# Optimization experiments

Hardware: AMD Instinct MI355X
Metric: run time of the kernel (lower is better)

Reference implementation:

```python
import jax, jax.numpy as jnp
import numpy as np

N = 50000
E = 800000
R = 8
F_IN = 128
H = 128          # num_hidden
F_OUT = 128      # num_outputs
D1, D2, D3 = 2 * H, H, F_OUT


def _glorot(key, shape):
    fan_in, fan_out = shape[-2], shape[-1]
    lim = np.sqrt(6.0 / (fan_in + fan_out)).astype(np.float32)
    return jax.random.uniform(key, shape, jnp.float32, -lim, lim)


def setup_inputs() -> dict:
    key = jax.random.key(0)
    ks = jax.random.split(key, 12)
    x = jax.random.normal(ks[0], (N, F_IN), jnp.float32)
    edge_index = jax.random.randint(ks[1], (2, E), 0, N, jnp.int64)
    edge_type = jax.random.randint(ks[2], (E,), 0, R, jnp.int64)
    return {
        "x": x,
        "edge_index": edge_index,
        "edge_type": edge_type,
        "w1": _glorot(ks[3], (R, F_IN, D1)),
        "root1": _glorot(ks[4], (F_IN, D1)),
        "b1": jnp.zeros((D1,), jnp.float32),
        "w2": _glorot(ks[5], (R, D1, D2)),
        "root2": _glorot(ks[6], (D1, D2)),
        "b2": jnp.zeros((D2,), jnp.float32),
        "w3": _glorot(ks[7], (R, D2, D3)),
        "root3": _glorot(ks[8], (D2, D3)),
        "b3": jnp.zeros((D3,), jnp.float32),
    }


def _rgcn_layer(h, src, dst, seg, inv_cnt, W, root, bias):
    # Per-relation mean aggregation via a fused (dst, rel) segment id,
    # then a grouped contraction with the per-relation weights.
    n, fin = h.shape
    s = jax.ops.segment_sum(h[src], seg, num_segments=n * R)  # [N*R, fin]
    agg = s.reshape(n, R, fin) * inv_cnt                      # mean per (node, rel)
    return jnp.einsum("nri,rio->no", agg, W) + h @ root + bias


def reference(x, edge_index, edge_type, w1, root1, b1, w2, root2, b2, w3, root3, b3):
    src, dst = edge_index[0], edge_index[1]
    seg = dst * R + edge_type                                  # fused (dst, rel) id
    cnt = jax.ops.segment_sum(jnp.ones((E,), x.dtype), seg, num_segments=N * R)
    inv_cnt = (1.0 / jnp.maximum(cnt, 1.0)).reshape(N, R, 1)

    h1 = jax.nn.elu(_rgcn_layer(x, src, dst, seg, inv_cnt, w1, root1, b1))
    # dropout: identity (eval mode)
    h2 = jax.nn.elu(_rgcn_layer(h1, src, dst, seg, inv_cnt, w2, root2, b2))
    h3 = jax.nn.elu(_rgcn_layer(h2, src, dst, seg, inv_cnt, w3, root3, b3))
    return jnp.concatenate([h1, h2, h3], axis=1)               # [N, D1+D2+D3]
```

## Files before the change

kernel.cpp:

```cpp
#include <hip/hip_runtime.h>


#define DEVI __device__ __forceinline__

constexpr int NN    = 50000;
constexpr int EE    = 800000;
constexpr int RREL  = 8;
constexpr int NRSEG = NN * RREL;
constexpr int NTC   = 1152;

using u16 = unsigned short;
using u32 = unsigned int;
using u64 = unsigned long long;

typedef short short8 __attribute__((ext_vector_type(8)));
typedef float f32x4  __attribute__((ext_vector_type(4)));

DEVI float bf2f(u32 u){ union{u32 i; float f;} x; x.i = u << 16; return x.f; }
DEVI u16   f2b(float f){ u32 u = __float_as_uint(f); u32 r = u + 0x7fffu + ((u >> 16) & 1u); return (u16)(r >> 16); }

typedef const __attribute__((address_space(1))) u32 gas_u32;
typedef __attribute__((address_space(3))) u32       las_u32;
DEVI void gload16(const void* g, void* l){
  __builtin_amdgcn_global_load_lds((gas_u32*)(u64)g, (las_u32*)(u64)l, 16, 0, 0);
}


__global__ void count_k(const int* __restrict__ dst, const int* __restrict__ et, int* __restrict__ cnt){
  int e = blockIdx.x * 256 + threadIdx.x;
  if(e < EE) atomicAdd(&cnt[dst[e] * RREL + et[e]], 1);
}

constexpr int SCAN_E = 8;
constexpr int CHUNK  = 2048;
constexpr int NB     = (NRSEG + CHUNK - 1) / CHUNK;

__global__ void scan1_k(const int* __restrict__ cnt, int* __restrict__ bsums){
  __shared__ int sm[256];
  int b = blockIdx.x, t = threadIdx.x;
  int base = b * CHUNK + t * SCAN_E;
  int s = 0;
  #pragma unroll
  for(int j = 0; j < SCAN_E; j++){ int i = base + j; s += (i < NRSEG) ? cnt[i] : 0; }
  sm[t] = s; __syncthreads();
  for(int off = 128; off > 0; off >>= 1){ if(t < off) sm[t] += sm[t + off]; __syncthreads(); }
  if(t == 0) bsums[b] = sm[0];
}

__global__ void scan2_k(int* __restrict__ bsums){
  __shared__ int sm[256];
  int t = threadIdx.x;
  int v = (t < NB) ? bsums[t] : 0;
  sm[t] = v; __syncthreads();
  for(int off = 1; off < 256; off <<= 1){
    int x = (t >= off) ? sm[t - off] : 0; __syncthreads();
    sm[t] += x; __syncthreads();
  }
  if(t < NB) bsums[t] = sm[t] - v;
}

__global__ void scan3_k(const int* __restrict__ cnt, const int* __restrict__ bsums, int* __restrict__ offs){
  __shared__ int sm[256];
  int b = blockIdx.x, t = threadIdx.x;
  int base = b * CHUNK + t * SCAN_E;
  int loc[SCAN_E]; int run = 0;
  #pragma unroll
  for(int j = 0; j < SCAN_E; j++){ int i = base + j; int c = (i < NRSEG) ? cnt[i] : 0; loc[j] = run; run += c; }
  sm[t] = run; __syncthreads();
  for(int off = 1; off < 256; off <<= 1){
    int x = (t >= off) ? sm[t - off] : 0; __syncthreads();
    sm[t] += x; __syncthreads();
  }
  int tb = bsums[b] + sm[t] - run;
  #pragma unroll
  for(int j = 0; j < SCAN_E; j++){ int i = base + j; if(i < NRSEG) offs[i] = tb + loc[j]; }
  if(b == 0 && t == 0) offs[NRSEG] = EE;
}

__global__ void inv_k(const int* __restrict__ cnt, float* __restrict__ inv){
  int i = blockIdx.x * 256 + threadIdx.x;
  if(i < NRSEG){ int c = cnt[i]; inv[i] = 1.0f / (float)(c > 0 ? c : 1); }
}

__global__ void fill_k(const int* __restrict__ src, const int* __restrict__ dst, const int* __restrict__ et,
                       const int* __restrict__ offs, int* __restrict__ fill, int* __restrict__ spk){
  int e = blockIdx.x * 256 + threadIdx.x;
  if(e < EE){
    int d = dst[e], r = et[e];
    int seg = d * RREL + r;
    int i = atomicAdd(&fill[seg], 1);
    spk[offs[seg] + i] = (src[e] << 3) | r;
  }
}

__global__ void castx_k(const float* __restrict__ x, u16* __restrict__ xb){
  int i = blockIdx.x * 256 + threadIdx.x;
  if(i < NN * 128) xb[i] = f2b(x[i]);
}

__global__ void packw_k(const float* __restrict__ w, const float* __restrict__ root,
                        u16* __restrict__ wp, int FIN, int FOUT){
  int idx = blockIdx.x * 256 + threadIdx.x;
  int tot = (RREL + 1) * FIN * FOUT;
  if(idx < tot){
    int i = idx % FIN;
    int o = (idx / FIN) % FOUT;
    int g = idx / (FIN * FOUT);
    float v = (g < RREL) ? w[((size_t)g * FIN + i) * FOUT + o] : root[(size_t)i * FOUT + o];
    wp[idx] = f2b(v);
  }
}


DEVI void acc8(float* a, uint4 v){
  a[0] += bf2f(v.x & 0xffffu); a[1] += bf2f(v.x >> 16);
  a[2] += bf2f(v.y & 0xffffu); a[3] += bf2f(v.y >> 16);
  a[4] += bf2f(v.z & 0xffffu); a[5] += bf2f(v.z >> 16);
  a[6] += bf2f(v.w & 0xffffu); a[7] += bf2f(v.w >> 16);
}

DEVI void fma8(float* a, uint4 v, float c){
  a[0] += c * bf2f(v.x & 0xffffu); a[1] += c * bf2f(v.x >> 16);
  a[2] += c * bf2f(v.y & 0xffffu); a[3] += c * bf2f(v.y >> 16);
  a[4] += c * bf2f(v.z & 0xffffu); a[5] += c * bf2f(v.z >> 16);
  a[6] += c * bf2f(v.w & 0xffffu); a[7] += c * bf2f(v.w >> 16);
}

template<int FIN, int RSUB>
__global__ __launch_bounds__(256)
void agg_k(const u16* __restrict__ hb, const int* __restrict__ spk,
           const int* __restrict__ offs, const float* __restrict__ inv,
           u16* __restrict__ agg, int r0)
{
  constexpr int G   = FIN / 8;
  constexpr int LDW = RSUB * FIN;
  const int gl  = threadIdx.x & (G - 1);
  int gid = (int)((blockIdx.x * blockDim.x + threadIdx.x) / G);
  const int ng = (int)((gridDim.x * blockDim.x) / G);
  const int S = NN * RSUB;
  for(int s = gid; s < S; s += ng){
    int n = s / RSUB, rr = s - n * RSUB;
    int seg = n * RREL + r0 + rr;
    int beg = offs[seg], end = offs[seg + 1];
    float sc = inv[seg];
    float acc[8];
    #pragma unroll
    for(int i = 0; i < 8; i++) acc[i] = 0.f;
    int e = beg;
    for(; e + 2 <= end; e += 2){
      int s0 = spk[e] >> 3, s1 = spk[e + 1] >> 3;
      uint4 v0 = ((const uint4*)(hb + (size_t)s0 * FIN))[gl];
      uint4 v1 = ((const uint4*)(hb + (size_t)s1 * FIN))[gl];
      acc8(acc, v0);
      acc8(acc, v1);
    }
    if(e < end){
      uint4 v0 = ((const uint4*)(hb + (size_t)(spk[e] >> 3) * FIN))[gl];
      acc8(acc, v0);
    }
    uint4 o;
    o.x = (u32)f2b(acc[0] * sc) | ((u32)f2b(acc[1] * sc) << 16);
    o.y = (u32)f2b(acc[2] * sc) | ((u32)f2b(acc[3] * sc) << 16);
    o.z = (u32)f2b(acc[4] * sc) | ((u32)f2b(acc[5] * sc) << 16);
    o.w = (u32)f2b(acc[6] * sc) | ((u32)f2b(acc[7] * sc) << 16);
    ((uint4*)(agg + (size_t)n * LDW + rr * FIN))[gl] = o;
  }
}


template<int FIN, int NAGG, bool ROOT, int FOUT>
__global__ __launch_bounds__(512)
void gemm_k(const u16* __restrict__ Aagg, const u16* __restrict__ Aroot,
            const u16* __restrict__ Wagg, const u16* __restrict__ Wroot,
            const float* __restrict__ bias, float* __restrict__ dout,
            u16* __restrict__ hbout)
{
  static_assert(FIN % 32 == 0, "");
  constexpr int KSG = FIN / 32;
  constexpr int NG  = NAGG + (ROOT ? 1 : 0);
  constexpr int NKS = NG * KSG;
  constexpr int LDA = NAGG * FIN;
  constexpr int WN    = (FOUT == 256) ? 4 : 2;
  constexpr int WM    = 8 / WN;
  constexpr int WROWS = 128 / WM;
  constexpr int MREP  = WROWS / 16;
  constexpr int ASL = 512;
  constexpr int BSL = FOUT * 4;
  __shared__ u16 lds[2][(ASL + BSL) * 8];
  const int bm  = (int)blockIdx.x;
  const int tid = threadIdx.x;
  const int wid = tid >> 6, lane = tid & 63;
  const int wm  = wid / WN, wn = wid % WN;

  auto stage = [&](int ks, u16* l){
    u16* lA = l;
    u16* lB = l + ASL * 8;
    int g    = ks / KSG;
    int koff = (ks - g * KSG) * 32;
    bool isRoot = ROOT && (g == NAGG);
    {
      int sb = wid * 64;
      int s  = sb + lane;
      int pair = s >> 3, cs = s & 7;
      int c    = cs ^ (pair & 7);
      int row  = pair * 2 + (c >> 2);
      int k8   = c & 3;
      int kk   = koff + k8 * 8;
      int rowg = bm * 128 + row; rowg = rowg < NN ? rowg : NN - 1;
      const u16* ga = isRoot ? (Aroot + (size_t)rowg * FIN + kk)
                             : (Aagg + (size_t)rowg * LDA + g * FIN + kk);
      gload16(ga, lA + sb * 8);
    }
    #pragma unroll
    for(int rnd = 0; rnd < BSL / 512; rnd++){
      int sb = rnd * 512 + wid * 64;
      int s  = sb + lane;
      int pair = s >> 3, cs = s & 7;
      int c    = cs ^ (pair & 7);
      int row  = pair * 2 + (c >> 2);
      int k8   = c & 3;
      int kk   = koff + k8 * 8;
      const u16* gb = isRoot ? (Wroot + (size_t)row * FIN + kk)
                             : (Wagg + ((size_t)g * FOUT + row) * FIN + kk);
      gload16(gb, lB + sb * 8);
    }
  };

  auto ldfrag = [&](const u16* buf, int row, int k8){
    int pair = row >> 1;
    int c    = ((row & 1) << 2) + k8;
    int cs   = c ^ (pair & 7);
    return *(const short8*)(buf + pair * 64 + cs * 8);
  };

  f32x4 acc[MREP][4] = {};

  stage(0, (u16*)lds[0]);
  __syncthreads();
  for(int ks = 0; ks < NKS; ks++){
    int cur = ks & 1;
    if(ks + 1 < NKS) stage(ks + 1, (u16*)lds[cur ^ 1]);
    const u16* lA = (const u16*)lds[cur];
    const u16* lB = lA + ASL * 8;
    short8 af[MREP], bf4[4];
    #pragma unroll
    for(int m = 0; m < MREP; m++) af[m] = ldfrag(lA, wm * WROWS + m * 16 + (lane & 15), lane >> 4);
    #pragma unroll
    for(int n = 0; n < 4; n++) bf4[n] = ldfrag(lB, wn * 64 + n * 16 + (lane & 15), lane >> 4);
    #pragma unroll
    for(int m = 0; m < MREP; m++)
      #pragma unroll
      for(int n = 0; n < 4; n++)
        acc[m][n] = __builtin_amdgcn_mfma_f32_16x16x32_bf16(af[m], bf4[n], acc[m][n], 0, 0, 0);
    __syncthreads();
  }

  #pragma unroll
  for(int m = 0; m < MREP; m++){
    #pragma unroll
    for(int j = 0; j < 4; j++){
      int grow = bm * 128 + wm * WROWS + m * 16 + (lane >> 4) * 4 + j;
      if(grow >= NN) continue;
      #pragma unroll
      for(int n = 0; n < 4; n++){
        int gcol = wn * 64 + n * 16 + (lane & 15);
        float v = acc[m][n][j];
        v += bias[gcol];
        v = v > 0.f ? v : expm1f(v);
        dout[(size_t)grow * 512 + gcol] = v;
        if(hbout) hbout[(size_t)grow * FOUT + gcol] = f2b(v);
      }
    }
  }
}


template<int FIN>
__global__ __launch_bounds__(512)
void dgemm_k(const u16* __restrict__ A, const u16* __restrict__ Bw, u16* __restrict__ T)
{
  constexpr int NKS = FIN / 32;
  constexpr int ASL = 512;
  constexpr int BSL = 512;
  constexpr int LPS = 2;
  __shared__ u16 lds[3][(ASL + BSL) * 8];
  const int bid = (int)blockIdx.x;
  const int bm  = bid / 9;
  const int jc  = bid % 9;
  const int tid = threadIdx.x;
  const int wid = tid >> 6, lane = tid & 63;
  const int wm  = wid >> 1, wn = wid & 1;

  auto stage = [&](int ks, u16* l){
    u16* lA = l;
    u16* lB = l + ASL * 8;
    int koff = ks * 32;
    {
      int sb = wid * 64;
      int s  = sb + lane;
      int pair = s >> 3, cs = s & 7;
      int c    = cs ^ (pair & 7);
      int row  = pair * 2 + (c >> 2);
      int k8   = c & 3;
      int kk   = koff + k8 * 8;
      int rowg = bm * 128 + row; rowg = rowg < NN ? rowg : NN - 1;
      gload16(A + (size_t)rowg * FIN + kk, lA + sb * 8);
    }
    {
      int sb = wid * 64;
      int s  = sb + lane;
      int pair = s >> 3, cs = s & 7;
      int c    = cs ^ (pair & 7);
      int row  = pair * 2 + (c >> 2);
      int k8   = c & 3;
      int kk   = koff + k8 * 8;
      gload16(Bw + ((size_t)(jc * 128 + row)) * FIN + kk, lB + sb * 8);
    }
  };

  auto ldfrag = [&](const u16* buf, int row, int k8){
    int pair = row >> 1;
    int c    = ((row & 1) << 2) + k8;
    int cs   = c ^ (pair & 7);
    return *(const short8*)(buf + pair * 64 + cs * 8);
  };

  f32x4 acc[2][4] = {};

  stage(0, (u16*)lds[0]);
  stage(1, (u16*)lds[1]);
  for(int ks = 0; ks < NKS; ks++){
    if(ks + 1 < NKS){
      asm volatile("s_waitcnt vmcnt(%0)" :: "i"(LPS) : "memory");
    } else {
      asm volatile("s_waitcnt vmcnt(0)" ::: "memory");
    }
    __builtin_amdgcn_sched_barrier(0);
    __builtin_amdgcn_s_barrier();
    __builtin_amdgcn_sched_barrier(0);
    if(ks + 2 < NKS) stage(ks + 2, (u16*)lds[(ks + 2) % 3]);
    const u16* lA = (const u16*)lds[ks % 3];
    const u16* lB = lA + ASL * 8;
    short8 af[2], bf4[4];
    #pragma unroll
    for(int m = 0; m < 2; m++) af[m] = ldfrag(lA, wm * 32 + m * 16 + (lane & 15), lane >> 4);
    #pragma unroll
    for(int n = 0; n < 4; n++) bf4[n] = ldfrag(lB, wn * 64 + n * 16 + (lane & 15), lane >> 4);
    #pragma unroll
    for(int m = 0; m < 2; m++)
      #pragma unroll
      for(int n = 0; n < 4; n++)
        acc[m][n] = __builtin_amdgcn_mfma_f32_16x16x32_bf16(af[m], bf4[n], acc[m][n], 0, 0, 0);
  }

  #pragma unroll
  for(int m = 0; m < 2; m++){
    #pragma unroll
    for(int j = 0; j < 4; j++){
      int grow = bm * 128 + wm * 32 + m * 16 + (lane >> 4) * 4 + j;
      if(grow >= NN) continue;
      #pragma unroll
      for(int n = 0; n < 4; n++){
        int gcol = wn * 64 + n * 16 + (lane & 15);
        T[(size_t)grow * NTC + jc * 128 + gcol] = f2b(acc[m][n][j]);
      }
    }
  }
}


template<bool HB>
__global__ __launch_bounds__(256)
void scat_k(const u16* __restrict__ T, const int* __restrict__ spk,
            const int* __restrict__ offs, const float* __restrict__ inv,
            const float* __restrict__ bias, float* __restrict__ dout, int dcol0,
            u16* __restrict__ hbout)
{
  const int gl = threadIdx.x & 15;
  int n = (int)((blockIdx.x * 256 + threadIdx.x) >> 4);
  if(n >= NN) return;
  const float* invn = inv + n * RREL;
  float acc[8];
  {
    uint4 v = *(const uint4*)(T + (size_t)n * NTC + 1024 + gl * 8);
    acc[0] = bf2f(v.x & 0xffffu); acc[1] = bf2f(v.x >> 16);
    acc[2] = bf2f(v.y & 0xffffu); acc[3] = bf2f(v.y >> 16);
    acc[4] = bf2f(v.z & 0xffffu); acc[5] = bf2f(v.z >> 16);
    acc[6] = bf2f(v.w & 0xffffu); acc[7] = bf2f(v.w >> 16);
  }
  int e  = offs[n * RREL];
  int e1 = offs[n * RREL + RREL];
  for(; e + 8 <= e1; e += 8){
    int p[8];
    #pragma unroll
    for(int j = 0; j < 8; j++) p[j] = spk[e + j];
    uint4 v[8];
    #pragma unroll
    for(int j = 0; j < 8; j++)
      v[j] = *(const uint4*)(T + (size_t)(p[j] >> 3) * NTC + (p[j] & 7) * 128 + gl * 8);
    #pragma unroll
    for(int j = 0; j < 8; j++) fma8(acc, v[j], invn[p[j] & 7]);
  }
  for(; e + 4 <= e1; e += 4){
    int p0 = spk[e], p1 = spk[e + 1], p2 = spk[e + 2], p3 = spk[e + 3];
    uint4 v0 = *(const uint4*)(T + (size_t)(p0 >> 3) * NTC + (p0 & 7) * 128 + gl * 8);
    uint4 v1 = *(const uint4*)(T + (size_t)(p1 >> 3) * NTC + (p1 & 7) * 128 + gl * 8);
    uint4 v2 = *(const uint4*)(T + (size_t)(p2 >> 3) * NTC + (p2 & 7) * 128 + gl * 8);
    uint4 v3 = *(const uint4*)(T + (size_t)(p3 >> 3) * NTC + (p3 & 7) * 128 + gl * 8);
    fma8(acc, v0, invn[p0 & 7]); fma8(acc, v1, invn[p1 & 7]);
    fma8(acc, v2, invn[p2 & 7]); fma8(acc, v3, invn[p3 & 7]);
  }
  for(; e < e1; e++){
    int p0 = spk[e];
    uint4 v0 = *(const uint4*)(T + (size_t)(p0 >> 3) * NTC + (p0 & 7) * 128 + gl * 8);
    fma8(acc, v0, invn[p0 & 7]);
  }
  float o[8];
  #pragma unroll
  for(int i = 0; i < 8; i++){
    float v = acc[i] + bias[gl * 8 + i];
    o[i] = v > 0.f ? v : expm1f(v);
  }
  float4* dp = (float4*)(dout + (size_t)n * 512 + dcol0 + gl * 8);
  dp[0] = make_float4(o[0], o[1], o[2], o[3]);
  dp[1] = make_float4(o[4], o[5], o[6], o[7]);
  if(HB){
    uint4 hv;
    hv.x = (u32)f2b(o[0]) | ((u32)f2b(o[1]) << 16);
    hv.y = (u32)f2b(o[2]) | ((u32)f2b(o[3]) << 16);
    hv.z = (u32)f2b(o[4]) | ((u32)f2b(o[5]) << 16);
    hv.w = (u32)f2b(o[6]) | ((u32)f2b(o[7]) << 16);
    *(uint4*)(hbout + (size_t)n * 128 + gl * 8) = hv;
  }
}


extern "C" void kernel_launch(void* const* d_in, const int* in_sizes, int n_in,
                              void* d_out, int out_size, void* d_ws, size_t ws_size,
                              hipStream_t stream)
{
  const float* x     = (const float*)d_in[0];
  const int*   ei    = (const int*)d_in[1];
  const int*   et    = (const int*)d_in[2];
  const float* w1    = (const float*)d_in[3];
  const float* root1 = (const float*)d_in[4];
  const float* b1    = (const float*)d_in[5];
  const float* w2    = (const float*)d_in[6];
  const float* root2 = (const float*)d_in[7];
  const float* b2    = (const float*)d_in[8];
  const float* w3    = (const float*)d_in[9];
  const float* root3 = (const float*)d_in[10];
  const float* b3    = (const float*)d_in[11];
  float* out = (float*)d_out;

  const int* esrc = ei;
  const int* edst = ei + EE;

  char* w = (char*)d_ws;
  auto alloc = [&](size_t bytes)->char*{ char* p = w; w += (bytes + 255) & ~(size_t)255; return p; };
  int*   cnt   = (int*)  alloc((size_t)NRSEG * 4);
  int*   offs  = (int*)  alloc((size_t)(NRSEG + 1) * 4);
  int*   fill  = (int*)  alloc((size_t)NRSEG * 4);
  float* inv   = (float*)alloc((size_t)NRSEG * 4);
  int*   spk   = (int*)  alloc((size_t)EE * 4);
  u16*   xb    = (u16*)  alloc((size_t)NN * 128 * 2);
  u16*   h1b   = (u16*)  alloc((size_t)NN * 256 * 2);
  u16*   h2b   = (u16*)  alloc((size_t)NN * 128 * 2);
  u16*   wp1   = (u16*)  alloc((size_t)9 * 256 * 128 * 2);
  u16*   wp2   = (u16*)  alloc((size_t)9 * 256 * 128 * 2);
  u16*   wp3   = (u16*)  alloc((size_t)9 * 128 * 128 * 2);
  int*   bsums = (int*)  alloc(1024 * 4);
  u16*   agg   = (u16*)  alloc((size_t)NN * 1024 * 2);
  u16*   T     = (u16*)  alloc((size_t)NN * NTC * 2);
  (void)ws_size; (void)in_sizes; (void)n_in; (void)out_size;

  hipMemsetAsync(cnt,  0, (size_t)NRSEG * 4, stream);
  hipMemsetAsync(fill, 0, (size_t)NRSEG * 4, stream);

  count_k<<<(EE + 255) / 256, 256, 0, stream>>>(edst, et, cnt);
  scan1_k<<<NB, 256, 0, stream>>>(cnt, bsums);
  scan2_k<<<1, 256, 0, stream>>>(bsums);
  scan3_k<<<NB, 256, 0, stream>>>(cnt, bsums, offs);
  inv_k<<<(NRSEG + 255) / 256, 256, 0, stream>>>(cnt, inv);
  fill_k<<<(EE + 255) / 256, 256, 0, stream>>>(esrc, edst, et, offs, fill, spk);
  castx_k<<<(NN * 128 + 255) / 256, 256, 0, stream>>>(x, xb);

  packw_k<<<(9 * 128 * 256 + 255) / 256, 256, 0, stream>>>(w1, root1, wp1, 128, 256);
  packw_k<<<(9 * 256 * 128 + 255) / 256, 256, 0, stream>>>(w2, root2, wp2, 256, 128);
  packw_k<<<(9 * 128 * 128 + 255) / 256, 256, 0, stream>>>(w3, root3, wp3, 128, 128);

  const int MT = (NN + 127) / 128;
  const int SB = (NN * 16 + 255) / 256;

  agg_k<128, 8><<<4096, 256, 0, stream>>>(xb, spk, offs, inv, agg, 0);
  gemm_k<128, 8, true, 256><<<MT, 512, 0, stream>>>(
      agg, xb, wp1, wp1 + (size_t)8 * 256 * 128, b1, out + 0, h1b);

  dgemm_k<256><<<MT * 9, 512, 0, stream>>>(h1b, wp2, T);
  scat_k<true><<<SB, 256, 0, stream>>>(T, spk, offs, inv, b2, out, 256, h2b);

  dgemm_k<128><<<MT * 9, 512, 0, stream>>>(h2b, wp3, T);
  scat_k<false><<<SB, 256, 0, stream>>>(T, spk, offs, inv, b3, out, 384, nullptr);
}
```

Before: 422.1 us.

## Fold root into aggregated buffer and reuse split-column dgemm for layer one

Layer one now packs the root features alongside the eight relation aggregates in a single K=1152 row buffer. Its weights are packed into one matching matrix. The dedicated full-width gemm kernel is replaced by the existing pipelined dgemm kernel, split into two 128-column blocks per row tile, with a bias/ELU epilogue. This raises the block count and uses the triple-buffered pipeline, at the cost of reading the A tile twice and an extra strided write of x into the aggregate buffer.

```diff
diff --git a/kernel.cpp b/kernel.cpp
--- a/kernel.cpp
+++ b/kernel.cpp
@@ -93,9 +93,14 @@
   }
 }
 
-__global__ void castx_k(const float* __restrict__ x, u16* __restrict__ xb){
+__global__ void castx_k(const float* __restrict__ x, u16* __restrict__ xb, u16* __restrict__ agg2){
   int i = blockIdx.x * 256 + threadIdx.x;
-  if(i < NN * 128) xb[i] = f2b(x[i]);
+  if(i < NN * 128){
+    u16 v = f2b(x[i]);
+    xb[i] = v;
+    int n = i >> 7, c = i & 127;
+    agg2[(size_t)n * NTC + 1024 + c] = v;
+  }
 }
 
 __global__ void packw_k(const float* __restrict__ w, const float* __restrict__ root,
@@ -111,6 +116,16 @@
   }
 }
 
+__global__ void packw1_k(const float* __restrict__ w, const float* __restrict__ root, u16* __restrict__ wp){
+  int idx = blockIdx.x * 256 + threadIdx.x;
+  if(idx < 256 * NTC){
+    int o = idx / NTC, k = idx % NTC;
+    int g = k >> 7, i = k & 127;
+    float v = (g < RREL) ? w[((size_t)g * 128 + i) * 256 + o] : root[(size_t)i * 256 + o];
+    wp[idx] = f2b(v);
+  }
+}
+
 
 DEVI void acc8(float* a, uint4 v){
   a[0] += bf2f(v.x & 0xffffu); a[1] += bf2f(v.x >> 16);
@@ -126,14 +141,13 @@
   a[6] += c * bf2f(v.w & 0xffffu); a[7] += c * bf2f(v.w >> 16);
 }
 
-template<int FIN, int RSUB>
+template<int FIN, int RSUB, int LDW>
 __global__ __launch_bounds__(256)
 void agg_k(const u16* __restrict__ hb, const int* __restrict__ spk,
            const int* __restrict__ offs, const float* __restrict__ inv,
            u16* __restrict__ agg, int r0)
 {
-  constexpr int G   = FIN / 8;
-  constexpr int LDW = RSUB * FIN;
+  constexpr int G = FIN / 8;
   const int gl  = threadIdx.x & (G - 1);
   int gid = (int)((blockIdx.x * blockDim.x + threadIdx.x) / G);
   const int ng = (int)((gridDim.x * blockDim.x) / G);
@@ -168,125 +182,20 @@
 }
 
 
-template<int FIN, int NAGG, bool ROOT, int FOUT>
+template<int K, int NJC, int EPI>
 __global__ __launch_bounds__(512)
-void gemm_k(const u16* __restrict__ Aagg, const u16* __restrict__ Aroot,
-            const u16* __restrict__ Wagg, const u16* __restrict__ Wroot,
-            const float* __restrict__ bias, float* __restrict__ dout,
-            u16* __restrict__ hbout)
+void dgemm_k(const u16* __restrict__ A, const u16* __restrict__ Bw,
+             u16* __restrict__ T, const float* __restrict__ bias,
+             float* __restrict__ dout, u16* __restrict__ hbout)
 {
-  static_assert(FIN % 32 == 0, "");
-  constexpr int KSG = FIN / 32;
-  constexpr int NG  = NAGG + (ROOT ? 1 : 0);
-  constexpr int NKS = NG * KSG;
-  constexpr int LDA = NAGG * FIN;
-  constexpr int WN    = (FOUT == 256) ? 4 : 2;
-  constexpr int WM    = 8 / WN;
-  constexpr int WROWS = 128 / WM;
-  constexpr int MREP  = WROWS / 16;
-  constexpr int ASL = 512;
-  constexpr int BSL = FOUT * 4;
-  __shared__ u16 lds[2][(ASL + BSL) * 8];
-  const int bm  = (int)blockIdx.x;
-  const int tid = threadIdx.x;
-  const int wid = tid >> 6, lane = tid & 63;
-  const int wm  = wid / WN, wn = wid % WN;
-
-  auto stage = [&](int ks, u16* l){
-    u16* lA = l;
-    u16* lB = l + ASL * 8;
-    int g    = ks / KSG;
-    int koff = (ks - g * KSG) * 32;
-    bool isRoot = ROOT && (g == NAGG);
-    {
-      int sb = wid * 64;
-      int s  = sb + lane;
-      int pair = s >> 3, cs = s & 7;
-      int c    = cs ^ (pair & 7);
-      int row  = pair * 2 + (c >> 2);
-      int k8   = c & 3;
-      int kk   = koff + k8 * 8;
-      int rowg = bm * 128 + row; rowg = rowg < NN ? rowg : NN - 1;
-      const u16* ga = isRoot ? (Aroot + (size_t)rowg * FIN + kk)
-                             : (Aagg + (size_t)rowg * LDA + g * FIN + kk);
-      gload16(ga, lA + sb * 8);
-    }
-    #pragma unroll
-    for(int rnd = 0; rnd < BSL / 512; rnd++){
-      int sb = rnd * 512 + wid * 64;
-      int s  = sb + lane;
-      int pair = s >> 3, cs = s & 7;
-      int c    = cs ^ (pair & 7);
-      int row  = pair * 2 + (c >> 2);
-      int k8   = c & 3;
-      int kk   = koff + k8 * 8;
-      const u16* gb = isRoot ? (Wroot + (size_t)row * FIN + kk)
-                             : (Wagg + ((size_t)g * FOUT + row) * FIN + kk);
-      gload16(gb, lB + sb * 8);
-    }
-  };
-
-  auto ldfrag = [&](const u16* buf, int row, int k8){
-    int pair = row >> 1;
-    int c    = ((row & 1) << 2) + k8;
-    int cs   = c ^ (pair & 7);
-    return *(const short8*)(buf + pair * 64 + cs * 8);
-  };
-
-  f32x4 acc[MREP][4] = {};
-
-  stage(0, (u16*)lds[0]);
-  __syncthreads();
-  for(int ks = 0; ks < NKS; ks++){
-    int cur = ks & 1;
-    if(ks + 1 < NKS) stage(ks + 1, (u16*)lds[cur ^ 1]);
-    const u16* lA = (const u16*)lds[cur];
-    const u16* lB = lA + ASL * 8;
-    short8 af[MREP], bf4[4];
-    #pragma unroll
-    for(int m = 0; m < MREP; m++) af[m] = ldfrag(lA, wm * WROWS + m * 16 + (lane & 15), lane >> 4);
-    #pragma unroll
-    for(int n = 0; n < 4; n++) bf4[n] = ldfrag(lB, wn * 64 + n * 16 + (lane & 15), lane >> 4);
-    #pragma unroll
-    for(int m = 0; m < MREP; m++)
-      #pragma unroll
-      for(int n = 0; n < 4; n++)
-        acc[m][n] = __builtin_amdgcn_mfma_f32_16x16x32_bf16(af[m], bf4[n], acc[m][n], 0, 0, 0);
-    __syncthreads();
-  }
-
-  #pragma unroll
-  for(int m = 0; m < MREP; m++){
-    #pragma unroll
-    for(int j = 0; j < 4; j++){
-      int grow = bm * 128 + wm * WROWS + m * 16 + (lane >> 4) * 4 + j;
-      if(grow >= NN) continue;
-      #pragma unroll
-      for(int n = 0; n < 4; n++){
-        int gcol = wn * 64 + n * 16 + (lane & 15);
-        float v = acc[m][n][j];
-        v += bias[gcol];
-        v = v > 0.f ? v : expm1f(v);
-        dout[(size_t)grow * 512 + gcol] = v;
-        if(hbout) hbout[(size_t)grow * FOUT + gcol] = f2b(v);
-      }
-    }
-  }
-}
-
-
-template<int FIN>
-__global__ __launch_bounds__(512)
-void dgemm_k(const u16* __restrict__ A, const u16* __restrict__ Bw, u16* __restrict__ T)
-{
-  constexpr int NKS = FIN / 32;
+  constexpr int NKS = K / 32;
   constexpr int ASL = 512;
   constexpr int BSL = 512;
   constexpr int LPS = 2;
   __shared__ u16 lds[3][(ASL + BSL) * 8];
   const int bid = (int)blockIdx.x;
-  const int bm  = bid / 9;
-  const int jc  = bid % 9;
+  const int bm  = bid / NJC;
+  const int jc  = bid % NJC;
   const int tid = threadIdx.x;
   const int wid = tid >> 6, lane = tid & 63;
   const int wm  = wid >> 1, wn = wid & 1;
@@ -304,7 +213,7 @@
       int k8   = c & 3;
       int kk   = koff + k8 * 8;
       int rowg = bm * 128 + row; rowg = rowg < NN ? rowg : NN - 1;
-      gload16(A + (size_t)rowg * FIN + kk, lA + sb * 8);
+      gload16(A + (size_t)rowg * K + kk, lA + sb * 8);
     }
     {
       int sb = wid * 64;
@@ -314,7 +223,7 @@
       int row  = pair * 2 + (c >> 2);
       int k8   = c & 3;
       int kk   = koff + k8 * 8;
-      gload16(Bw + ((size_t)(jc * 128 + row)) * FIN + kk, lB + sb * 8);
+      gload16(Bw + ((size_t)(jc * 128 + row)) * K + kk, lB + sb * 8);
     }
   };
 
@@ -361,8 +270,16 @@
       if(grow >= NN) continue;
       #pragma unroll
       for(int n = 0; n < 4; n++){
-        int gcol = wn * 64 + n * 16 + (lane & 15);
-        T[(size_t)grow * NTC + jc * 128 + gcol] = f2b(acc[m][n][j]);
+        int lcol = wn * 64 + n * 16 + (lane & 15);
+        if constexpr(EPI == 0){
+          T[(size_t)grow * NTC + jc * 128 + lcol] = f2b(acc[m][n][j]);
+        } else {
+          int gcol = jc * 128 + lcol;
+          float v = acc[m][n][j] + bias[gcol];
+          v = v > 0.f ? v : expm1f(v);
+          dout[(size_t)grow * 512 + gcol] = v;
+          hbout[(size_t)grow * 256 + gcol] = f2b(v);
+        }
       }
     }
   }
@@ -466,11 +383,11 @@
   u16*   xb    = (u16*)  alloc((size_t)NN * 128 * 2);
   u16*   h1b   = (u16*)  alloc((size_t)NN * 256 * 2);
   u16*   h2b   = (u16*)  alloc((size_t)NN * 128 * 2);
-  u16*   wp1   = (u16*)  alloc((size_t)9 * 256 * 128 * 2);
+  u16*   wpL1  = (u16*)  alloc((size_t)256 * NTC * 2);
   u16*   wp2   = (u16*)  alloc((size_t)9 * 256 * 128 * 2);
   u16*   wp3   = (u16*)  alloc((size_t)9 * 128 * 128 * 2);
   int*   bsums = (int*)  alloc(1024 * 4);
-  u16*   agg   = (u16*)  alloc((size_t)NN * 1024 * 2);
+  u16*   agg2  = (u16*)  alloc((size_t)NN * NTC * 2);
   u16*   T     = (u16*)  alloc((size_t)NN * NTC * 2);
   (void)ws_size; (void)in_sizes; (void)n_in; (void)out_size;
 
@@ -483,22 +400,21 @@
   scan3_k<<<NB, 256, 0, stream>>>(cnt, bsums, offs);
   inv_k<<<(NRSEG + 255) / 256, 256, 0, stream>>>(cnt, inv);
   fill_k<<<(EE + 255) / 256, 256, 0, stream>>>(esrc, edst, et, offs, fill, spk);
-  castx_k<<<(NN * 128 + 255) / 256, 256, 0, stream>>>(x, xb);
-
-  packw_k<<<(9 * 128 * 256 + 255) / 256, 256, 0, stream>>>(w1, root1, wp1, 128, 256);
+  castx_k<<<(NN * 128 + 255) / 256, 256, 0, stream>>>(x, xb, agg2);
+
+  packw1_k<<<(256 * NTC + 255) / 256, 256, 0, stream>>>(w1, root1, wpL1);
   packw_k<<<(9 * 256 * 128 + 255) / 256, 256, 0, stream>>>(w2, root2, wp2, 256, 128);
   packw_k<<<(9 * 128 * 128 + 255) / 256, 256, 0, stream>>>(w3, root3, wp3, 128, 128);
 
   const int MT = (NN + 127) / 128;
   const int SB = (NN * 16 + 255) / 256;
 
-  agg_k<128, 8><<<4096, 256, 0, stream>>>(xb, spk, offs, inv, agg, 0);
-  gemm_k<128, 8, true, 256><<<MT, 512, 0, stream>>>(
-      agg, xb, wp1, wp1 + (size_t)8 * 256 * 128, b1, out + 0, h1b);
-
-  dgemm_k<256><<<MT * 9, 512, 0, stream>>>(h1b, wp2, T);
+  agg_k<128, 8, NTC><<<4096, 256, 0, stream>>>(xb, spk, offs, inv, agg2, 0);
+  dgemm_k<NTC, 2, 1><<<MT * 2, 512, 0, stream>>>(agg2, wpL1, nullptr, b1, out, h1b);
+
+  dgemm_k<256, 9, 0><<<MT * 9, 512, 0, stream>>>(h1b, wp2, T, nullptr, nullptr, nullptr);
   scat_k<true><<<SB, 256, 0, stream>>>(T, spk, offs, inv, b2, out, 256, h2b);
 
-  dgemm_k<128><<<MT * 9, 512, 0, stream>>>(h2b, wp3, T);
+  dgemm_k<128, 9, 0><<<MT * 9, 512, 0, stream>>>(h2b, wp3, T, nullptr, nullptr, nullptr);
   scat_k<false><<<SB, 256, 0, stream>>>(T, spk, offs, inv, b3, out, 384, nullptr);
 }
```

Measured after the change: 434.9 us. 3.0% more time.
